# Kernel optimization log

Hardware: AMD Instinct MI355X
Metric: run time of the kernel (lower is better)

## Reference

```python
import jax, jax.numpy as jnp
import numpy as np

B, HG, WG, D, NH, K = 4, 32, 32, 768, 12, 7
HD = D // NH  # 64


def _neigh_idx(H, W, k):
    # NATTEN semantics: 7x7 window centered at the query, shifted (clamped)
    # at borders so every query has exactly k*k neighbors.
    si = np.clip(np.arange(H) - k // 2, 0, H - k)  # [H] window row starts
    sj = np.clip(np.arange(W) - k // 2, 0, W - k)  # [W] window col starts
    ri = si[:, None] + np.arange(k)[None, :]       # [H, k]
    cj = sj[:, None] + np.arange(k)[None, :]       # [W, k]
    idx = ri[:, None, :, None] * W + cj[None, :, None, :]  # [H, W, k, k]
    return jnp.asarray(idx.reshape(H * W, k * k), dtype=jnp.int32)


def setup_inputs() -> dict:
    key = jax.random.key(0)
    ks = jax.random.split(key, 3)
    s = D ** -0.5
    return {
        "x": jax.random.normal(ks[0], (B, HG * WG, D), dtype=jnp.float32),
        "qkv_w": jax.random.normal(ks[1], (3 * D, D), dtype=jnp.float32) * s,
        "qkv_b": jnp.zeros((3 * D,), dtype=jnp.float32),
        "proj_w": jax.random.normal(ks[2], (D, D), dtype=jnp.float32) * s,
        "proj_b": jnp.zeros((D,), dtype=jnp.float32),
    }


def reference(x, qkv_w, qkv_b, proj_w, proj_b):
    b, n, d = x.shape  # n == HG*WG
    idx = _neigh_idx(HG, WG, K)  # [n, K*K] flat neighbor token indices

    qkv = x @ qkv_w.T + qkv_b                      # [b, n, 3d]
    q, k, v = jnp.split(qkv, 3, axis=-1)
    q = q.reshape(b, n, NH, HD) * (HD ** -0.5)     # [b, n, h, hd]
    k = k.reshape(b, n, NH, HD)
    v = v.reshape(b, n, NH, HD)

    kn = jnp.take(k, idx, axis=1)                  # [b, n, 49, h, hd]
    vn = jnp.take(v, idx, axis=1)                  # [b, n, 49, h, hd]

    scores = jnp.einsum('bnhd,bnkhd->bnhk', q, kn)  # [b, n, h, 49]
    attn = jax.nn.softmax(scores, axis=-1)
    out = jnp.einsum('bnhk,bnkhd->bnhd', attn, vn).reshape(b, n, d)
    return out @ proj_w.T + proj_b
```

## Files before the change

kernel.cpp:

```cpp
#include <hip/hip_runtime.h>


typedef __bf16 bf16x8 __attribute__((ext_vector_type(8)));
typedef short s16x4 __attribute__((ext_vector_type(4)));
typedef float f32x4 __attribute__((ext_vector_type(4)));

__device__ __forceinline__ unsigned short f2bf(float f) {
  unsigned u = __float_as_uint(f);
  u += 0x7fffu + ((u >> 16) & 1u);
  return (unsigned short)(u >> 16);
}

template <typename T>
__device__ __forceinline__ void gld_lds16(const T* g, T* l) {
  __builtin_amdgcn_global_load_lds((const __attribute__((address_space(1))) void*)g,
                                   (__attribute__((address_space(3))) void*)l, 16, 0, 0);
}

__global__ void cvt_kernel(const float* __restrict__ x, const float* __restrict__ w1,
                           const float* __restrict__ w2, unsigned short* __restrict__ xo,
                           unsigned short* __restrict__ w1o, unsigned short* __restrict__ w2o) {
  const int n1 = 4096 * 768 / 4;
  const int n2 = 2304 * 768 / 4;
  const int n3 = 768 * 768 / 4;
  int i = blockIdx.x * 256 + threadIdx.x;
  float4 v;
  unsigned short* dst;
  int o;
  if (i < n1) {
    o = i; v = ((const float4*)x)[o]; dst = xo;
  } else if (i < n1 + n2) {
    o = i - n1; v = ((const float4*)w1)[o]; dst = w1o;
  } else if (i < n1 + n2 + n3) {
    o = i - n1 - n2; v = ((const float4*)w2)[o]; dst = w2o;
  } else {
    return;
  }
  ushort4 r;
  r.x = f2bf(v.x); r.y = f2bf(v.y); r.z = f2bf(v.z); r.w = f2bf(v.w);
  ((ushort4*)dst)[o] = r;
}

__global__ __launch_bounds__(512, 2) void gemm_qkv8(const unsigned short* __restrict__ A,
                                                    const unsigned short* __restrict__ Bm,
                                                    const float* __restrict__ bias,
                                                    unsigned short* __restrict__ obf,
                                                    unsigned short* __restrict__ vtout) {
  __shared__ __align__(16) unsigned short sA[2][256 * 64];
  __shared__ __align__(16) unsigned short sB[2][256 * 64];
  const int tid = threadIdx.x, lane = tid & 63, wv = tid >> 6;
  const int wr = wv >> 2, wc = wv & 3;
  const int lr = lane & 15, lq = lane >> 4;

  const int lin = blockIdx.x;
  const int wgid = (lin & 7) * 18 + (lin >> 3);
  const int bx = wgid % 9, by = wgid / 9;
  const int m0 = by * 256, n0 = bx * 256;

  const int srow = tid >> 3;
  const int sc8 = (tid & 7) * 8;
  const int scl8 = (((tid & 7) ^ ((tid >> 3) & 7))) * 8;
  const unsigned short* gA = A + (size_t)(m0 + srow) * 768 + scl8;
  const unsigned short* gB = Bm + (size_t)(n0 + srow) * 768 + scl8;
  const int ldst = srow * 64 + sc8;

  f32x4 acc[8][4] = {};

#define STG(t, p)                                                                     \
  do {                                                                                \
    unsigned short* dA = sA[(t) & 1];                                                 \
    unsigned short* dB = sB[(t) & 1];                                                 \
    const int ko = (t) * 64;                                                          \
    gld_lds16(gA + (size_t)((p) * 128) * 768 + ko, dA + ((p) * 128) * 64 + ldst);     \
    gld_lds16(gA + (size_t)((p) * 128 + 64) * 768 + ko, dA + ((p) * 128 + 64) * 64 + ldst); \
    gld_lds16(gB + (size_t)((p) * 128) * 768 + ko, dB + ((p) * 128) * 64 + ldst);     \
    gld_lds16(gB + (size_t)((p) * 128 + 64) * 768 + ko, dB + ((p) * 128 + 64) * 64 + ldst); \
  } while (0)

  STG(0, 0);
  STG(0, 1);
  __builtin_amdgcn_sched_barrier(0);
  asm volatile("s_waitcnt vmcnt(0) lgkmcnt(0)" ::: "memory");
  __builtin_amdgcn_s_barrier();

  for (int t = 0; t < 12; ++t) {
    const unsigned short* cA = sA[t & 1];
    const unsigned short* cB = sB[t & 1];
    bf16x8 bfr[4][2];
#pragma unroll
    for (int nf = 0; nf < 4; ++nf)
#pragma unroll
      for (int ks = 0; ks < 2; ++ks)
        bfr[nf][ks] = *(const bf16x8*)(cB + (wc * 64 + nf * 16 + lr) * 64 +
                                       (((ks * 4 + lq) ^ (lr & 7)) << 3));
#pragma unroll
    for (int ph = 0; ph < 4; ++ph) {
      bf16x8 af[2][2];
#pragma unroll
      for (int i = 0; i < 2; ++i)
#pragma unroll
        for (int ks = 0; ks < 2; ++ks)
          af[i][ks] = *(const bf16x8*)(cA + (wr * 128 + (ph * 2 + i) * 16 + lr) * 64 +
                                       (((ks * 4 + lq) ^ (lr & 7)) << 3));
      if (ph < 2 && t + 1 < 12) STG(t + 1, ph);
      __builtin_amdgcn_s_barrier();
      __builtin_amdgcn_s_setprio(1);
#pragma unroll
      for (int i = 0; i < 2; ++i)
#pragma unroll
        for (int nf = 0; nf < 4; ++nf)
#pragma unroll
          for (int ks = 0; ks < 2; ++ks)
            acc[ph * 2 + i][nf] = __builtin_amdgcn_mfma_f32_16x16x32_bf16(
                af[i][ks], bfr[nf][ks], acc[ph * 2 + i][nf], 0, 0, 0);
      __builtin_amdgcn_s_setprio(0);
      if (ph == 3) {
        __builtin_amdgcn_sched_barrier(0);
        if (t + 1 < 12) asm volatile("s_waitcnt vmcnt(0)" ::: "memory");
      }
      __builtin_amdgcn_s_barrier();
    }
  }
#undef STG

  const int sidx = n0 / 768;
  if (sidx == 2) {
#pragma unroll
    for (int mf = 0; mf < 8; ++mf) {
#pragma unroll
      for (int nf = 0; nf < 4; ++nf) {
        int gn = n0 + wc * 64 + nf * 16 + lr;
        int rem = gn - 1536;
        int hh = rem >> 6, dd = gn & 63;
        float bsv = bias[gn];
        int gm0 = m0 + wr * 128 + mf * 16 + lq * 4;
        ushort4 pk;
        pk.x = f2bf(acc[mf][nf][0] + bsv);
        pk.y = f2bf(acc[mf][nf][1] + bsv);
        pk.z = f2bf(acc[mf][nf][2] + bsv);
        pk.w = f2bf(acc[mf][nf][3] + bsv);
        *(ushort4*)(vtout + (size_t)(hh * 64 + dd) * 4096 + gm0) = pk;
      }
    }
  } else {
    const float scale = (sidx == 0) ? 0.18033688f : 1.0f;
#pragma unroll
    for (int mf = 0; mf < 8; ++mf) {
#pragma unroll
      for (int nf = 0; nf < 4; ++nf) {
        int gn = n0 + wc * 64 + nf * 16 + lr;
        int rem = gn - sidx * 768;
        int hh = rem >> 6, dd = gn & 63;
        float bsv = bias[gn];
#pragma unroll
        for (int r = 0; r < 4; ++r) {
          int gm = m0 + wr * 128 + mf * 16 + lq * 4 + r;
          float val = (acc[mf][nf][r] + bsv) * scale;
          obf[((size_t)(sidx * 12 + hh) * 4096 + gm) * 64 + dd] = f2bf(val);
        }
      }
    }
  }
}

template <int MODE, int BM, int BN>
__global__ __launch_bounds__(256) void gemm_bt(const unsigned short* __restrict__ A,
                                               const unsigned short* __restrict__ Bm,
                                               const float* __restrict__ bias,
                                               unsigned short* __restrict__ obf,
                                               unsigned short* __restrict__ vtout,
                                               float* __restrict__ of32,
                                               int M, int N, int Kd) {
  constexpr int RA = BM / 64, RB = BN / 64;
  constexpr int MI = BM / 32, NI = BN / 32;
  constexpr int NB = (MODE == 0) ? 4 : 5;
  constexpr int DEPTH = NB - 1;
  __shared__ __align__(16) unsigned short sA[NB][BM * 32];
  __shared__ __align__(16) unsigned short sB[NB][BN * 32];
  const int tid = threadIdx.x;
  const int lane = tid & 63;
  const int wv = tid >> 6;

  constexpr int HX = (MODE == 0) ? 9 : 6;
  constexpr int HY = (MODE == 0) ? 8 : 16;
  const int lin = blockIdx.y * gridDim.x + blockIdx.x;
  const int xcd = lin & 7, rrr = lin >> 3;
  const int bx = (xcd & 1) * HX + rrr % HX;
  const int by = (xcd >> 1) * HY + rrr / HX;
  const int m0 = by * BM, n0 = bx * BN;

  const int wrow = (wv >> 1) * (BM / 2), wcol = (wv & 1) * (BN / 2);
  const int lr = lane & 15, lq = lane >> 4;
  const int rchunk = (lq ^ ((lr >> 1) & 3)) * 8;

  f32x4 acc[MI][NI] = {};

  const int schunk = ((tid & 3) ^ ((tid >> 3) & 3)) * 8;
  const unsigned short* gA = A + (size_t)(m0 + (tid >> 2)) * Kd + schunk;
  const unsigned short* gB = Bm + (size_t)(n0 + (tid >> 2)) * Kd + schunk;

  const int NS = Kd >> 5;

#define STAGE_TILE(tile, bufidx)                                                          \
  do {                                                                                    \
    const int _off = (tile) * 32;                                                         \
    unsigned short* _dA = sA[(bufidx)];                                                   \
    unsigned short* _dB = sB[(bufidx)];                                                   \
    _Pragma("unroll")                                                                     \
    for (int _r = 0; _r < RA; ++_r)                                                       \
      gld_lds16(gA + (size_t)(_r * 64) * Kd + _off, _dA + _r * 2048 + tid * 8);           \
    _Pragma("unroll")                                                                     \
    for (int _r = 0; _r < RB; ++_r)                                                       \
      gld_lds16(gB + (size_t)(_r * 64) * Kd + _off, _dB + _r * 2048 + tid * 8);           \
  } while (0)

#pragma unroll
  for (int t = 0; t < DEPTH; ++t) STAGE_TILE(t, t);
  __builtin_amdgcn_sched_barrier(0);
  if constexpr (MODE == 0) asm volatile("s_waitcnt vmcnt(8) lgkmcnt(0)" ::: "memory");
  else                     asm volatile("s_waitcnt vmcnt(6) lgkmcnt(0)" ::: "memory");
  __builtin_amdgcn_s_barrier();

  int rb = 0, sb = DEPTH;
  for (int step = 0; step < NS; ++step) {
    const unsigned short* cA = sA[rb];
    const unsigned short* cB = sB[rb];
    bf16x8 af[MI], bfr[NI];
#pragma unroll
    for (int t = 0; t < MI; ++t) af[t] = *(const bf16x8*)(cA + (wrow + t * 16 + lr) * 32 + rchunk);
#pragma unroll
    for (int t = 0; t < NI; ++t) bfr[t] = *(const bf16x8*)(cB + (wcol + t * 16 + lr) * 32 + rchunk);

    if (step + DEPTH < NS) STAGE_TILE(step + DEPTH, sb);

#pragma unroll
    for (int im = 0; im < MI; ++im)
#pragma unroll
      for (int in = 0; in < NI; ++in)
        acc[im][in] = __builtin_amdgcn_mfma_f32_16x16x32_bf16(af[im], bfr[in], acc[im][in], 0, 0, 0);

    __builtin_amdgcn_sched_barrier(0);
    if constexpr (MODE == 0) {
      if (step + 3 < NS)      asm volatile("s_waitcnt vmcnt(8) lgkmcnt(0)" ::: "memory");
      else if (step + 2 < NS) asm volatile("s_waitcnt vmcnt(4) lgkmcnt(0)" ::: "memory");
      else                    asm volatile("s_waitcnt vmcnt(0) lgkmcnt(0)" ::: "memory");
    } else {
      if (step + 4 < NS)      asm volatile("s_waitcnt vmcnt(6) lgkmcnt(0)" ::: "memory");
      else if (step + 3 < NS) asm volatile("s_waitcnt vmcnt(4) lgkmcnt(0)" ::: "memory");
      else if (step + 2 < NS) asm volatile("s_waitcnt vmcnt(2) lgkmcnt(0)" ::: "memory");
      else                    asm volatile("s_waitcnt vmcnt(0) lgkmcnt(0)" ::: "memory");
    }
    __builtin_amdgcn_s_barrier();
    rb = (rb + 1 == NB) ? 0 : rb + 1;
    sb = (sb + 1 == NB) ? 0 : sb + 1;
  }
#undef STAGE_TILE

  if (MODE == 0) {
  } else {
#pragma unroll
    for (int im = 0; im < MI; ++im) {
#pragma unroll
      for (int in = 0; in < NI; ++in) {
        int gn = n0 + wcol + in * 16 + lr;
        float bsv = bias[gn];
#pragma unroll
        for (int r = 0; r < 4; ++r) {
          int gm = m0 + wrow + im * 16 + lq * 4 + r;
          of32[(size_t)gm * N + gn] = acc[im][in][r] + bsv;
        }
      }
    }
  }
}

__global__ __launch_bounds__(256, 2) void natten_kernel(const unsigned short* __restrict__ qkvt,
                                                        unsigned short* __restrict__ aout) {
  __shared__ __align__(16) unsigned short sQ[64 * 64];
  __shared__ __align__(16) unsigned short sK[256 * 64];
  __shared__ __align__(16) unsigned short sVt[64 * 256];
  const int h = blockIdx.x, ip = blockIdx.y, b = blockIdx.z;
  const int i0 = ip * 2;
  const int tid = threadIdx.x, lane = tid & 63, wv = tid >> 6;
  const int lg = lane >> 4, lm = lane & 15;
  int si0 = i0 - 3; si0 = si0 < 0 ? 0 : si0; if (si0 > 25) si0 = 25;
  const int gb = b * 1024;
  const unsigned short* Qg = qkvt + ((size_t)h * 4096 + gb + i0 * 32) * 64;
  const unsigned short* Kg = qkvt + ((size_t)(12 + h) * 4096 + gb) * 64;
  const unsigned short* Vg = qkvt + (size_t)24 * 4096 * 64 + (size_t)h * 64 * 4096 + gb;

#pragma unroll
  for (int it = 0; it < 2; ++it) {
    int f = it * 256 + tid;
    int q = f >> 3, c16 = f & 7;
    uint4 v = *(const uint4*)(Qg + q * 64 + c16 * 8);
    int s = q & 15;
    *(uint2*)(sQ + q * 64 + ((((c16 << 1)) ^ s) << 2)) = make_uint2(v.x, v.y);
    *(uint2*)(sQ + q * 64 + ((((c16 << 1) | 1) ^ s) << 2)) = make_uint2(v.z, v.w);
  }
#pragma unroll
  for (int it = 0; it < 8; ++it) {
    int f = it * 256 + tid;
    int t = f >> 3, c16 = f & 7;
    int wr = t >> 5, c = t & 31;
    int row = si0 + wr; if (row > 31) row = 31;
    uint4 v = *(const uint4*)(Kg + (row * 32 + c) * 64 + c16 * 8);
    int s = t & 15;
    *(uint2*)(sK + t * 64 + ((((c16 << 1)) ^ s) << 2)) = make_uint2(v.x, v.y);
    *(uint2*)(sK + t * 64 + ((((c16 << 1) | 1) ^ s) << 2)) = make_uint2(v.z, v.w);
  }
#pragma unroll
  for (int it = 0; it < 8; ++it) {
    int f = it * 256 + tid;
    int d = f >> 5, tc16 = f & 31;
    int wr = tc16 >> 2;
    int row = si0 + wr; if (row > 31) row = 31;
    uint4 v = *(const uint4*)(Vg + (size_t)d * 4096 + row * 32 + (tc16 & 3) * 8);
    int s = d & 15;
    *(uint2*)(sVt + d * 256 + ((((tc16 << 1)) ^ s) << 2)) = make_uint2(v.x, v.y);
    *(uint2*)(sVt + d * 256 + ((((tc16 << 1) | 1) ^ s) << 2)) = make_uint2(v.z, v.w);
  }
  __syncthreads();

  const int row_sel = wv >> 1;
  const int jhalf = wv & 1;
  const int i = i0 + row_sel;
  int si_w = i - 3; si_w = si_w < 0 ? 0 : si_w; if (si_w > 25) si_w = 25;
  const int toff = (si_w - si0) * 32;
  const int j = jhalf * 16 + lm;
  int sj = j - 3; sj = sj < 0 ? 0 : sj; if (sj > 25) sj = 25;

  float madd[2][4];
#pragma unroll
  for (int p = 0; p < 2; ++p)
#pragma unroll
    for (int r = 0; r < 4; ++r) {
      int c = p * 16 + lg * 4 + r;
      madd[p][r] = (c >= sj && c <= sj + 6) ? 0.f : -1e30f;
    }

  s16x4 qf[4];
  const int qrow = row_sel * 32 + j;
#pragma unroll
  for (int ks = 0; ks < 4; ++ks)
    qf[ks] = *(const s16x4*)(sQ + qrow * 64 + ((((ks << 2) + lg) ^ (qrow & 15)) << 2));

  f32x4 accS[14];
#pragma unroll
  for (int tt = 0; tt < 14; ++tt) {
    f32x4 a = {0.f, 0.f, 0.f, 0.f};
    const int trow = toff + tt * 16 + lm;
    const unsigned short* kr = sK + trow * 64;
    const int sw = trow & 15;
#pragma unroll
    for (int ks = 0; ks < 4; ++ks) {
      s16x4 kf = *(const s16x4*)(kr + ((((ks << 2) + lg) ^ sw) << 2));
      a = __builtin_amdgcn_mfma_f32_16x16x16bf16_1k(kf, qf[ks], a, 0, 0, 0);
    }
    accS[tt] = a;
  }

  float mx = -3e38f;
#pragma unroll
  for (int tt = 0; tt < 14; ++tt)
#pragma unroll
    for (int r = 0; r < 4; ++r) {
      float v = accS[tt][r] + madd[tt & 1][r];
      accS[tt][r] = v;
      mx = fmaxf(mx, v);
    }
  mx = fmaxf(mx, __shfl_xor(mx, 16, 64));
  mx = fmaxf(mx, __shfl_xor(mx, 32, 64));
  float sum = 0.f;
#pragma unroll
  for (int tt = 0; tt < 14; ++tt)
#pragma unroll
    for (int r = 0; r < 4; ++r) {
      float p = exp2f(accS[tt][r] - mx);
      accS[tt][r] = p;
      sum += p;
    }
  sum += __shfl_xor(sum, 16, 64);
  sum += __shfl_xor(sum, 32, 64);
  const float inv = 1.f / sum;

  s16x4 pf[14];
#pragma unroll
  for (int tt = 0; tt < 14; ++tt) {
    union { unsigned u[2]; s16x4 v; } pk;
    pk.u[0] = ((unsigned)f2bf(accS[tt][1]) << 16) | f2bf(accS[tt][0]);
    pk.u[1] = ((unsigned)f2bf(accS[tt][3]) << 16) | f2bf(accS[tt][2]);
    pf[tt] = pk.v;
  }

  f32x4 accO[4] = {};
  const int choff = toff >> 2;
#pragma unroll
  for (int tt = 0; tt < 14; ++tt) {
    const int c8 = choff + tt * 4 + lg;
#pragma unroll
    for (int nt = 0; nt < 4; ++nt) {
      const int d = nt * 16 + lm;
      s16x4 vf = *(const s16x4*)(sVt + d * 256 + ((c8 ^ (d & 15)) << 2));
      accO[nt] = __builtin_amdgcn_mfma_f32_16x16x16bf16_1k(pf[tt], vf, accO[nt], 0, 0, 0);
    }
  }

  float invr[4];
#pragma unroll
  for (int r = 0; r < 4; ++r) invr[r] = __shfl(inv, lg * 4 + r, 64);

  const int tokbase = gb + i * 32 + jhalf * 16;
#pragma unroll
  for (int nt = 0; nt < 4; ++nt)
#pragma unroll
    for (int r = 0; r < 4; ++r) {
      int tok = tokbase + lg * 4 + r;
      aout[(size_t)tok * 768 + h * 64 + nt * 16 + lm] = f2bf(accO[nt][r] * invr[r]);
    }
}

extern "C" void kernel_launch(void* const* d_in, const int* in_sizes, int n_in,
                              void* d_out, int out_size, void* d_ws, size_t ws_size,
                              hipStream_t stream) {
  const float* x      = (const float*)d_in[0];
  const float* qkv_w  = (const float*)d_in[1];
  const float* qkv_b  = (const float*)d_in[2];
  const float* proj_w = (const float*)d_in[3];
  const float* proj_b = (const float*)d_in[4];
  char* ws = (char*)d_ws;

  unsigned short* xb    = (unsigned short*)(ws);
  unsigned short* wqkv  = (unsigned short*)(ws + 6291456);
  unsigned short* wproj = (unsigned short*)(ws + 9830400);
  unsigned short* qkvt  = (unsigned short*)(ws + 11010048);
  unsigned short* attnb = (unsigned short*)(ws + 29884416);
  unsigned short* vt    = qkvt + (size_t)24 * 4096 * 64;
  float* out = (float*)d_out;

  cvt_kernel<<<5376, 256, 0, stream>>>(x, qkv_w, proj_w, xb, wqkv, wproj);
  gemm_qkv8<<<144, 512, 0, stream>>>(xb, wqkv, qkv_b, qkvt, vt);
  natten_kernel<<<dim3(12, 16, 4), 256, 0, stream>>>(qkvt, attnb);
  gemm_bt<1, 64, 64><<<dim3(12, 64), 256, 0, stream>>>(attnb, wproj, proj_b, nullptr, nullptr, out, 4096, 768, 768);
}
```

Before: 136.5 us.

## Fuse all four stages into one cooperative persistent kernel with grid syncs

Replaces the four separate launches (convert, QKV GEMM, neighborhood attention, projection GEMM) with one cooperative kernel of 256 blocks of 512 threads. The phases are separated by grid.sync and share a union of LDS buffers. Each block runs two 256-thread units per pass. The attention phase now reads Q fragments straight from global memory instead of staging them in LDS. This is meant to remove launch gaps and tail effects between kernels. In exchange it pays for grid-wide barriers, keeps only 144 of 256 blocks busy in the QKV phase, and runs a second pass per block with half the threads idle.

After: 392.7 us. 2.88x slower.

```diff
diff --git a/kernel.cpp b/kernel.cpp
--- a/kernel.cpp
+++ b/kernel.cpp
@@ -1,4 +1,7 @@
 #include <hip/hip_runtime.h>
+#include <hip/hip_cooperative_groups.h>
+
+namespace cg = cooperative_groups;
 
 
 typedef __bf16 bf16x8 __attribute__((ext_vector_type(8)));
@@ -17,43 +20,48 @@
                                    (__attribute__((address_space(3))) void*)l, 16, 0, 0);
 }
 
-__global__ void cvt_kernel(const float* __restrict__ x, const float* __restrict__ w1,
-                           const float* __restrict__ w2, unsigned short* __restrict__ xo,
-                           unsigned short* __restrict__ w1o, unsigned short* __restrict__ w2o) {
+union Smem {
+  struct { unsigned short a[2][256 * 64]; unsigned short b[2][256 * 64]; } g;
+  struct { unsigned short k[2][256 * 64]; unsigned short v[2][64 * 256]; } n;
+  struct { unsigned short a[2][5][64 * 32]; unsigned short b[2][5][64 * 32]; } p;
+};
+
+__device__ __forceinline__ void cvt_phase(int gid, int gstride,
+                                          const float* __restrict__ x, const float* __restrict__ w1,
+                                          const float* __restrict__ w2, unsigned short* __restrict__ xo,
+                                          unsigned short* __restrict__ w1o, unsigned short* __restrict__ w2o) {
   const int n1 = 4096 * 768 / 4;
   const int n2 = 2304 * 768 / 4;
   const int n3 = 768 * 768 / 4;
-  int i = blockIdx.x * 256 + threadIdx.x;
-  float4 v;
-  unsigned short* dst;
-  int o;
-  if (i < n1) {
-    o = i; v = ((const float4*)x)[o]; dst = xo;
-  } else if (i < n1 + n2) {
-    o = i - n1; v = ((const float4*)w1)[o]; dst = w1o;
-  } else if (i < n1 + n2 + n3) {
-    o = i - n1 - n2; v = ((const float4*)w2)[o]; dst = w2o;
-  } else {
-    return;
-  }
-  ushort4 r;
-  r.x = f2bf(v.x); r.y = f2bf(v.y); r.z = f2bf(v.z); r.w = f2bf(v.w);
-  ((ushort4*)dst)[o] = r;
-}
-
-__global__ __launch_bounds__(512, 2) void gemm_qkv8(const unsigned short* __restrict__ A,
-                                                    const unsigned short* __restrict__ Bm,
-                                                    const float* __restrict__ bias,
-                                                    unsigned short* __restrict__ obf,
-                                                    unsigned short* __restrict__ vtout) {
-  __shared__ __align__(16) unsigned short sA[2][256 * 64];
-  __shared__ __align__(16) unsigned short sB[2][256 * 64];
-  const int tid = threadIdx.x, lane = tid & 63, wv = tid >> 6;
+  for (int i = gid; i < n1 + n2 + n3; i += gstride) {
+    float4 v;
+    unsigned short* dst;
+    int o;
+    if (i < n1) {
+      o = i; v = ((const float4*)x)[o]; dst = xo;
+    } else if (i < n1 + n2) {
+      o = i - n1; v = ((const float4*)w1)[o]; dst = w1o;
+    } else {
+      o = i - n1 - n2; v = ((const float4*)w2)[o]; dst = w2o;
+    }
+    ushort4 r;
+    r.x = f2bf(v.x); r.y = f2bf(v.y); r.z = f2bf(v.z); r.w = f2bf(v.w);
+    ((ushort4*)dst)[o] = r;
+  }
+}
+
+__device__ __forceinline__ void qkv_tile(int tid, int bid,
+                                         unsigned short (*sA)[256 * 64], unsigned short (*sB)[256 * 64],
+                                         const unsigned short* __restrict__ A,
+                                         const unsigned short* __restrict__ Bm,
+                                         const float* __restrict__ bias,
+                                         unsigned short* __restrict__ obf,
+                                         unsigned short* __restrict__ vtout) {
+  const int lane = tid & 63, wv = tid >> 6;
   const int wr = wv >> 2, wc = wv & 3;
   const int lr = lane & 15, lq = lane >> 4;
 
-  const int lin = blockIdx.x;
-  const int wgid = (lin & 7) * 18 + (lin >> 3);
+  const int wgid = (bid & 7) * 18 + (bid >> 3);
   const int bx = wgid % 9, by = wgid / 9;
   const int m0 = by * 256, n0 = bx * 256;
 
@@ -66,15 +74,15 @@
 
   f32x4 acc[8][4] = {};
 
-#define STG(t, p)                                                                     \
-  do {                                                                                \
-    unsigned short* dA = sA[(t) & 1];                                                 \
-    unsigned short* dB = sB[(t) & 1];                                                 \
-    const int ko = (t) * 64;                                                          \
-    gld_lds16(gA + (size_t)((p) * 128) * 768 + ko, dA + ((p) * 128) * 64 + ldst);     \
-    gld_lds16(gA + (size_t)((p) * 128 + 64) * 768 + ko, dA + ((p) * 128 + 64) * 64 + ldst); \
-    gld_lds16(gB + (size_t)((p) * 128) * 768 + ko, dB + ((p) * 128) * 64 + ldst);     \
-    gld_lds16(gB + (size_t)((p) * 128 + 64) * 768 + ko, dB + ((p) * 128 + 64) * 64 + ldst); \
+#define STG(t, p)                                                                            \
+  do {                                                                                       \
+    unsigned short* dA = sA[(t) & 1];                                                        \
+    unsigned short* dB = sB[(t) & 1];                                                        \
+    const int ko = (t) * 64;                                                                 \
+    gld_lds16(gA + (size_t)((p) * 128) * 768 + ko, dA + ((p) * 128) * 64 + ldst);            \
+    gld_lds16(gA + (size_t)((p) * 128 + 64) * 768 + ko, dA + ((p) * 128 + 64) * 64 + ldst);  \
+    gld_lds16(gB + (size_t)((p) * 128) * 768 + ko, dB + ((p) * 128) * 64 + ldst);            \
+    gld_lds16(gB + (size_t)((p) * 128 + 64) * 768 + ko, dB + ((p) * 128 + 64) * 64 + ldst);  \
   } while (0)
 
   STG(0, 0);
@@ -163,141 +171,22 @@
   }
 }
 
-template <int MODE, int BM, int BN>
-__global__ __launch_bounds__(256) void gemm_bt(const unsigned short* __restrict__ A,
-                                               const unsigned short* __restrict__ Bm,
-                                               const float* __restrict__ bias,
-                                               unsigned short* __restrict__ obf,
-                                               unsigned short* __restrict__ vtout,
-                                               float* __restrict__ of32,
-                                               int M, int N, int Kd) {
-  constexpr int RA = BM / 64, RB = BN / 64;
-  constexpr int MI = BM / 32, NI = BN / 32;
-  constexpr int NB = (MODE == 0) ? 4 : 5;
-  constexpr int DEPTH = NB - 1;
-  __shared__ __align__(16) unsigned short sA[NB][BM * 32];
-  __shared__ __align__(16) unsigned short sB[NB][BN * 32];
-  const int tid = threadIdx.x;
-  const int lane = tid & 63;
-  const int wv = tid >> 6;
-
-  constexpr int HX = (MODE == 0) ? 9 : 6;
-  constexpr int HY = (MODE == 0) ? 8 : 16;
-  const int lin = blockIdx.y * gridDim.x + blockIdx.x;
-  const int xcd = lin & 7, rrr = lin >> 3;
-  const int bx = (xcd & 1) * HX + rrr % HX;
-  const int by = (xcd >> 1) * HY + rrr / HX;
-  const int m0 = by * BM, n0 = bx * BN;
-
-  const int wrow = (wv >> 1) * (BM / 2), wcol = (wv & 1) * (BN / 2);
-  const int lr = lane & 15, lq = lane >> 4;
-  const int rchunk = (lq ^ ((lr >> 1) & 3)) * 8;
-
-  f32x4 acc[MI][NI] = {};
-
-  const int schunk = ((tid & 3) ^ ((tid >> 3) & 3)) * 8;
-  const unsigned short* gA = A + (size_t)(m0 + (tid >> 2)) * Kd + schunk;
-  const unsigned short* gB = Bm + (size_t)(n0 + (tid >> 2)) * Kd + schunk;
-
-  const int NS = Kd >> 5;
-
-#define STAGE_TILE(tile, bufidx)                                                          \
-  do {                                                                                    \
-    const int _off = (tile) * 32;                                                         \
-    unsigned short* _dA = sA[(bufidx)];                                                   \
-    unsigned short* _dB = sB[(bufidx)];                                                   \
-    _Pragma("unroll")                                                                     \
-    for (int _r = 0; _r < RA; ++_r)                                                       \
-      gld_lds16(gA + (size_t)(_r * 64) * Kd + _off, _dA + _r * 2048 + tid * 8);           \
-    _Pragma("unroll")                                                                     \
-    for (int _r = 0; _r < RB; ++_r)                                                       \
-      gld_lds16(gB + (size_t)(_r * 64) * Kd + _off, _dB + _r * 2048 + tid * 8);           \
-  } while (0)
-
-#pragma unroll
-  for (int t = 0; t < DEPTH; ++t) STAGE_TILE(t, t);
-  __builtin_amdgcn_sched_barrier(0);
-  if constexpr (MODE == 0) asm volatile("s_waitcnt vmcnt(8) lgkmcnt(0)" ::: "memory");
-  else                     asm volatile("s_waitcnt vmcnt(6) lgkmcnt(0)" ::: "memory");
-  __builtin_amdgcn_s_barrier();
-
-  int rb = 0, sb = DEPTH;
-  for (int step = 0; step < NS; ++step) {
-    const unsigned short* cA = sA[rb];
-    const unsigned short* cB = sB[rb];
-    bf16x8 af[MI], bfr[NI];
-#pragma unroll
-    for (int t = 0; t < MI; ++t) af[t] = *(const bf16x8*)(cA + (wrow + t * 16 + lr) * 32 + rchunk);
-#pragma unroll
-    for (int t = 0; t < NI; ++t) bfr[t] = *(const bf16x8*)(cB + (wcol + t * 16 + lr) * 32 + rchunk);
-
-    if (step + DEPTH < NS) STAGE_TILE(step + DEPTH, sb);
-
-#pragma unroll
-    for (int im = 0; im < MI; ++im)
-#pragma unroll
-      for (int in = 0; in < NI; ++in)
-        acc[im][in] = __builtin_amdgcn_mfma_f32_16x16x32_bf16(af[im], bfr[in], acc[im][in], 0, 0, 0);
-
-    __builtin_amdgcn_sched_barrier(0);
-    if constexpr (MODE == 0) {
-      if (step + 3 < NS)      asm volatile("s_waitcnt vmcnt(8) lgkmcnt(0)" ::: "memory");
-      else if (step + 2 < NS) asm volatile("s_waitcnt vmcnt(4) lgkmcnt(0)" ::: "memory");
-      else                    asm volatile("s_waitcnt vmcnt(0) lgkmcnt(0)" ::: "memory");
-    } else {
-      if (step + 4 < NS)      asm volatile("s_waitcnt vmcnt(6) lgkmcnt(0)" ::: "memory");
-      else if (step + 3 < NS) asm volatile("s_waitcnt vmcnt(4) lgkmcnt(0)" ::: "memory");
-      else if (step + 2 < NS) asm volatile("s_waitcnt vmcnt(2) lgkmcnt(0)" ::: "memory");
-      else                    asm volatile("s_waitcnt vmcnt(0) lgkmcnt(0)" ::: "memory");
-    }
-    __builtin_amdgcn_s_barrier();
-    rb = (rb + 1 == NB) ? 0 : rb + 1;
-    sb = (sb + 1 == NB) ? 0 : sb + 1;
-  }
-#undef STAGE_TILE
-
-  if (MODE == 0) {
-  } else {
-#pragma unroll
-    for (int im = 0; im < MI; ++im) {
-#pragma unroll
-      for (int in = 0; in < NI; ++in) {
-        int gn = n0 + wcol + in * 16 + lr;
-        float bsv = bias[gn];
-#pragma unroll
-        for (int r = 0; r < 4; ++r) {
-          int gm = m0 + wrow + im * 16 + lq * 4 + r;
-          of32[(size_t)gm * N + gn] = acc[im][in][r] + bsv;
-        }
-      }
-    }
-  }
-}
-
-__global__ __launch_bounds__(256, 2) void natten_kernel(const unsigned short* __restrict__ qkvt,
-                                                        unsigned short* __restrict__ aout) {
-  __shared__ __align__(16) unsigned short sQ[64 * 64];
-  __shared__ __align__(16) unsigned short sK[256 * 64];
-  __shared__ __align__(16) unsigned short sVt[64 * 256];
-  const int h = blockIdx.x, ip = blockIdx.y, b = blockIdx.z;
+__device__ __forceinline__ void natten_unit(int tid, unsigned short* sK, unsigned short* sVt,
+                                            const unsigned short* __restrict__ qkvt,
+                                            unsigned short* __restrict__ aout,
+                                            int u, bool valid) {
+  const int h = u % 12;
+  const int rr = u / 12;
+  const int ip = rr & 15, bz = rr >> 4;
   const int i0 = ip * 2;
-  const int tid = threadIdx.x, lane = tid & 63, wv = tid >> 6;
+  const int lane = tid & 63, wv = tid >> 6;
   const int lg = lane >> 4, lm = lane & 15;
   int si0 = i0 - 3; si0 = si0 < 0 ? 0 : si0; if (si0 > 25) si0 = 25;
-  const int gb = b * 1024;
+  const int gb = bz * 1024;
   const unsigned short* Qg = qkvt + ((size_t)h * 4096 + gb + i0 * 32) * 64;
   const unsigned short* Kg = qkvt + ((size_t)(12 + h) * 4096 + gb) * 64;
   const unsigned short* Vg = qkvt + (size_t)24 * 4096 * 64 + (size_t)h * 64 * 4096 + gb;
 
-#pragma unroll
-  for (int it = 0; it < 2; ++it) {
-    int f = it * 256 + tid;
-    int q = f >> 3, c16 = f & 7;
-    uint4 v = *(const uint4*)(Qg + q * 64 + c16 * 8);
-    int s = q & 15;
-    *(uint2*)(sQ + q * 64 + ((((c16 << 1)) ^ s) << 2)) = make_uint2(v.x, v.y);
-    *(uint2*)(sQ + q * 64 + ((((c16 << 1) | 1) ^ s) << 2)) = make_uint2(v.z, v.w);
-  }
 #pragma unroll
   for (int it = 0; it < 8; ++it) {
     int f = it * 256 + tid;
@@ -343,7 +232,7 @@
   const int qrow = row_sel * 32 + j;
 #pragma unroll
   for (int ks = 0; ks < 4; ++ks)
-    qf[ks] = *(const s16x4*)(sQ + qrow * 64 + ((((ks << 2) + lg) ^ (qrow & 15)) << 2));
+    qf[ks] = *(const s16x4*)(Qg + qrow * 64 + ks * 16 + lg * 4);
 
   f32x4 accS[14];
 #pragma unroll
@@ -410,14 +299,136 @@
 #pragma unroll
   for (int r = 0; r < 4; ++r) invr[r] = __shfl(inv, lg * 4 + r, 64);
 
-  const int tokbase = gb + i * 32 + jhalf * 16;
-#pragma unroll
-  for (int nt = 0; nt < 4; ++nt)
-#pragma unroll
-    for (int r = 0; r < 4; ++r) {
-      int tok = tokbase + lg * 4 + r;
-      aout[(size_t)tok * 768 + h * 64 + nt * 16 + lm] = f2bf(accO[nt][r] * invr[r]);
-    }
+  if (valid) {
+    const int tokbase = gb + i * 32 + jhalf * 16;
+#pragma unroll
+    for (int nt = 0; nt < 4; ++nt)
+#pragma unroll
+      for (int r = 0; r < 4; ++r) {
+        int tok = tokbase + lg * 4 + r;
+        aout[(size_t)tok * 768 + h * 64 + nt * 16 + lm] = f2bf(accO[nt][r] * invr[r]);
+      }
+  }
+}
+
+__device__ __forceinline__ void proj_unit(int t2, unsigned short (*sAu)[64 * 32], unsigned short (*sBu)[64 * 32],
+                                          const unsigned short* __restrict__ A,
+                                          const unsigned short* __restrict__ Bm,
+                                          const float* __restrict__ bias,
+                                          float* __restrict__ of32,
+                                          int m0, int n0, bool valid) {
+  const int lane = t2 & 63, wv = t2 >> 6;
+  const int wrow = (wv >> 1) * 32, wcol = (wv & 1) * 32;
+  const int lr = lane & 15, lq = lane >> 4;
+  const int rchunk = (lq ^ ((lr >> 1) & 3)) * 8;
+  f32x4 acc[2][2] = {};
+  const int schunk = ((t2 & 3) ^ ((t2 >> 3) & 3)) * 8;
+  const unsigned short* gA = A + (size_t)(m0 + (t2 >> 2)) * 768 + schunk;
+  const unsigned short* gB = Bm + (size_t)(n0 + (t2 >> 2)) * 768 + schunk;
+
+  asm volatile("s_waitcnt vmcnt(0)" ::: "memory");
+
+#define PSTG(tile, buf)                               \
+  do {                                                \
+    gld_lds16(gA + (tile) * 32, sAu[(buf)] + t2 * 8); \
+    gld_lds16(gB + (tile) * 32, sBu[(buf)] + t2 * 8); \
+  } while (0)
+
+#pragma unroll
+  for (int t = 0; t < 4; ++t) PSTG(t, t);
+  __builtin_amdgcn_sched_barrier(0);
+  asm volatile("s_waitcnt vmcnt(6) lgkmcnt(0)" ::: "memory");
+  __builtin_amdgcn_s_barrier();
+
+  int rb = 0, sb = 4;
+  for (int step = 0; step < 24; ++step) {
+    const unsigned short* cA = sAu[rb];
+    const unsigned short* cB = sBu[rb];
+    bf16x8 af[2], bfr[2];
+#pragma unroll
+    for (int t = 0; t < 2; ++t) af[t] = *(const bf16x8*)(cA + (wrow + t * 16 + lr) * 32 + rchunk);
+#pragma unroll
+    for (int t = 0; t < 2; ++t) bfr[t] = *(const bf16x8*)(cB + (wcol + t * 16 + lr) * 32 + rchunk);
+    if (step + 4 < 24) PSTG(step + 4, sb);
+#pragma unroll
+    for (int im = 0; im < 2; ++im)
+#pragma unroll
+      for (int in = 0; in < 2; ++in)
+        acc[im][in] = __builtin_amdgcn_mfma_f32_16x16x32_bf16(af[im], bfr[in], acc[im][in], 0, 0, 0);
+    __builtin_amdgcn_sched_barrier(0);
+    if (step + 4 < 24)      asm volatile("s_waitcnt vmcnt(6) lgkmcnt(0)" ::: "memory");
+    else if (step + 3 < 24) asm volatile("s_waitcnt vmcnt(4) lgkmcnt(0)" ::: "memory");
+    else if (step + 2 < 24) asm volatile("s_waitcnt vmcnt(2) lgkmcnt(0)" ::: "memory");
+    else                    asm volatile("s_waitcnt vmcnt(0) lgkmcnt(0)" ::: "memory");
+    __builtin_amdgcn_s_barrier();
+    rb = (rb + 1 == 5) ? 0 : rb + 1;
+    sb = (sb + 1 == 5) ? 0 : sb + 1;
+  }
+#undef PSTG
+
+  if (valid) {
+#pragma unroll
+    for (int im = 0; im < 2; ++im)
+#pragma unroll
+      for (int in = 0; in < 2; ++in) {
+        int gn = n0 + wcol + in * 16 + lr;
+        float bsv = bias[gn];
+#pragma unroll
+        for (int r = 0; r < 4; ++r) {
+          int gm = m0 + wrow + im * 16 + lq * 4 + r;
+          of32[(size_t)gm * 768 + gn] = acc[im][in][r] + bsv;
+        }
+      }
+  }
+}
+
+__global__ __launch_bounds__(512, 2) void mega(const float* __restrict__ x,
+                                               const float* __restrict__ qkv_w,
+                                               const float* __restrict__ qkv_b,
+                                               const float* __restrict__ proj_w,
+                                               const float* __restrict__ proj_b,
+                                               unsigned short* __restrict__ xb,
+                                               unsigned short* __restrict__ wqkv,
+                                               unsigned short* __restrict__ wproj,
+                                               unsigned short* __restrict__ qkvt,
+                                               unsigned short* __restrict__ vt,
+                                               unsigned short* __restrict__ attnb,
+                                               float* __restrict__ out) {
+  __shared__ Smem sm;
+  const int tid = threadIdx.x;
+  const int bid = blockIdx.x;
+  cg::grid_group grid = cg::this_grid();
+
+  cvt_phase(bid * 512 + tid, 256 * 512, x, qkv_w, proj_w, xb, wqkv, wproj);
+  __threadfence();
+  grid.sync();
+
+  if (bid < 144) qkv_tile(tid, bid, sm.g.a, sm.g.b, xb, wqkv, qkv_b, qkvt, vt);
+  __threadfence();
+  grid.sync();
+
+  {
+    const int sub = tid >> 8, t2 = tid & 255;
+    for (int pass = 0; pass < 2; ++pass) {
+      if (pass) __syncthreads();
+      const int u = 3 * bid + (pass == 0 ? sub : 2);
+      const bool valid = (pass == 0) || (sub == 0);
+      natten_unit(t2, sm.n.k[sub], sm.n.v[sub], qkvt, attnb, u, valid);
+    }
+  }
+  __threadfence();
+  grid.sync();
+
+  {
+    const int sub = tid >> 8, t2 = tid & 255;
+    for (int pass = 0; pass < 2; ++pass) {
+      if (pass) __syncthreads();
+      const int t = 3 * bid + (pass == 0 ? sub : 2);
+      const bool valid = (pass == 0) || (sub == 0);
+      proj_unit(t2, sm.p.a[sub], sm.p.b[sub], attnb, wproj, proj_b, out,
+                (t / 12) * 64, (t % 12) * 64, valid);
+    }
+  }
 }
 
 extern "C" void kernel_launch(void* const* d_in, const int* in_sizes, int n_in,
@@ -438,8 +449,8 @@
   unsigned short* vt    = qkvt + (size_t)24 * 4096 * 64;
   float* out = (float*)d_out;
 
-  cvt_kernel<<<5376, 256, 0, stream>>>(x, qkv_w, proj_w, xb, wqkv, wproj);
-  gemm_qkv8<<<144, 512, 0, stream>>>(xb, wqkv, qkv_b, qkvt, vt);
-  natten_kernel<<<dim3(12, 16, 4), 256, 0, stream>>>(qkvt, attnb);
-  gemm_bt<1, 64, 64><<<dim3(12, 64), 256, 0, stream>>>(attnb, wproj, proj_b, nullptr, nullptr, out, 4096, 768, 768);
-}
+  void* kargs[] = {(void*)&x, (void*)&qkv_w, (void*)&qkv_b, (void*)&proj_w, (void*)&proj_b,
+                   (void*)&xb, (void*)&wqkv, (void*)&wproj, (void*)&qkvt, (void*)&vt,
+                   (void*)&attnb, (void*)&out};
+  hipLaunchCooperativeKernel((const void*)mega, dim3(256), dim3(512), kargs, 0, stream);
+}
```
